# Kernel tuning notes

Measured on AMD Instinct MI355X. Metric: run time of the kernel, lower is better.

The kernel has to match this reference:

```python
import jax, jax.numpy as jnp
import numpy as np

B, L, D, H = 2, 2048, 1024, 16
DH = D // H  # 64

def setup_inputs() -> dict:
    key = jax.random.key(0)
    ks = jax.random.split(key, 5)
    s = 1.0 / np.sqrt(D)
    return {
        "x": jax.random.normal(ks[0], (B, L, D), jnp.float32),
        "Wk": jax.random.normal(ks[1], (D, D), jnp.float32) * s,
        "Wq": jax.random.normal(ks[2], (D, D), jnp.float32) * s,
        "Wv": jax.random.normal(ks[3], (D, D), jnp.float32) * s,
        "Wo": jax.random.normal(ks[4], (D, D), jnp.float32) * s,
    }

def reference(x, Wk, Wq, Wv, Wo):
    # Linear(D,D,bias=False): y = x @ W.T ; W stored [out,in] as in torch
    k = (x @ Wk.T).reshape(B, L, H, DH).transpose(0, 2, 1, 3)  # [B,H,L,dh]
    q = (x @ Wq.T).reshape(B, L, H, DH).transpose(0, 2, 1, 3)
    v = (x @ Wv.T).reshape(B, L, H, DH).transpose(0, 2, 1, 3)
    att = jnp.einsum("bhqd,bhkd->bhqk", q, k) / jnp.sqrt(jnp.float32(DH))
    causal = jnp.tril(jnp.ones((L, L), dtype=bool))
    att = jnp.where(causal, att, -jnp.inf)
    p = jax.nn.softmax(att, axis=-1)  # dropout omitted (eval mode)
    out = jnp.einsum("bhqk,bhkd->bhqd", p, v)  # [B,H,L,dh]
    out = out.transpose(0, 2, 1, 3).reshape(B, L, D)
    return out @ Wo.T
```

## Files before the change

### kernel.cpp

```cpp
#include <hip/hip_runtime.h>

typedef __bf16 bf16_t;
typedef __bf16 bf16x8 __attribute__((ext_vector_type(8)));
typedef __bf16 bf16x4 __attribute__((ext_vector_type(4)));
typedef float f32x4 __attribute__((ext_vector_type(4)));

#define MFMA_BF16(a, b, c) __builtin_amdgcn_mfma_f32_16x16x32_bf16((a), (b), (c), 0, 0, 0)
#define LOG2E 1.44269504088896f

__device__ __forceinline__ void gload16(const bf16_t* g, bf16_t* l) {
  __builtin_amdgcn_global_load_lds(
      (__attribute__((address_space(1))) void*)(g),
      (__attribute__((address_space(3))) void*)(l), 16, 0, 0);
}

__global__ void cast_all(const float* __restrict__ x, const float* __restrict__ wk,
                         const float* __restrict__ wq, const float* __restrict__ wv,
                         const float* __restrict__ wo, bf16_t* __restrict__ xbf,
                         bf16_t* __restrict__ wbf) {
  const size_t NX = 4194304, NW = 1048576;
  size_t i = (size_t)blockIdx.x * blockDim.x + threadIdx.x;
  const size_t total4 = (NX + 4 * NW) / 4;
  const size_t stride = (size_t)gridDim.x * blockDim.x;
  for (; i < total4; i += stride) {
    size_t f = i * 4;
    const float* src;
    bf16_t* dst;
    if (f < NX) {
      src = x + f;
      dst = xbf + f;
    } else {
      size_t g = f - NX;
      size_t wsel = g >> 20;
      size_t off = g & (NW - 1);
      dst = wbf + g;
      src = (wsel == 0) ? wq + off : (wsel == 1) ? wk + off : (wsel == 2) ? wv + off : wo + off;
    }
    float4 v = *(const float4*)src;
    bf16x4 o;
    o[0] = (bf16_t)v.x; o[1] = (bf16_t)v.y; o[2] = (bf16_t)v.z; o[3] = (bf16_t)v.w;
    *(bf16x4*)dst = o;
  }
}

template <int BM, int BN, typename TOUT>
__global__ __launch_bounds__(256) void gemm_nt(const bf16_t* __restrict__ A,
                                               const bf16_t* __restrict__ W,
                                               TOUT* __restrict__ C, int K, int ldc,
                                               int blocksPerSect, bf16_t* __restrict__ vtb) {
  constexpr int MF = BM / 32;
  constexpr int NF = BN / 32;
  __shared__ bf16_t As[BM * 32];
  __shared__ bf16_t Bs[BN * 32];
  const int t = threadIdx.x;
  const int l = t & 63, w = t >> 6;
  const int wm = w >> 1;
  const int wn = w & 1;
  const int lr = l & 15, lg = l >> 4;
  const int bm = blockIdx.x;
  const int by = blockIdx.y;
  const int sect = by / blocksPerSect;
  const int bn = by - sect * blocksPerSect;
  const bf16_t* Wp = W + ((size_t)sect << 20);
  const int n0 = sect * 1024 + bn * BN;

  const bf16_t* ag = A + (size_t)(bm * BM + (t >> 2)) * K + (t & 3) * 8;
  const bf16_t* bg = Wp + (size_t)(bn * BN + (t >> 2)) * K + (t & 3) * 8;
  const size_t rs64 = (size_t)64 * K;

  f32x4 acc[MF][NF];
#pragma unroll
  for (int i = 0; i < MF; ++i)
#pragma unroll
    for (int j = 0; j < NF; ++j) acc[i][j] = (f32x4){0.f, 0.f, 0.f, 0.f};

  for (int k0 = 0; k0 < K; k0 += 32) {
    __syncthreads();
    gload16(ag, As + t * 8);
    if (BM == 128) gload16(ag + rs64, As + 2048 + t * 8);
    gload16(bg, Bs + t * 8);
    if (BN == 128) gload16(bg + rs64, Bs + 2048 + t * 8);
    ag += 32;
    bg += 32;
    __syncthreads();
    bf16x8 af[MF], bfr[NF];
#pragma unroll
    for (int mf = 0; mf < MF; ++mf)
      af[mf] = *(const bf16x8*)(As + (wm * (MF * 16) + mf * 16 + lr) * 32 + lg * 8);
#pragma unroll
    for (int nf = 0; nf < NF; ++nf)
      bfr[nf] = *(const bf16x8*)(Bs + (wn * (NF * 16) + nf * 16 + lr) * 32 + lg * 8);
#pragma unroll
    for (int mf = 0; mf < MF; ++mf)
#pragma unroll
      for (int nf = 0; nf < NF; ++nf)
        acc[mf][nf] = MFMA_BF16(af[mf], bfr[nf], acc[mf][nf]);
  }

  if constexpr (BM == 128 && BN == 128) {
    if (vtb != nullptr && sect == 2) {
#pragma unroll
      for (int mf = 0; mf < MF; ++mf)
#pragma unroll
        for (int nf = 0; nf < NF; ++nf) {
          int row0 = bm * 128 + wm * 64 + mf * 16 + lg * 4;
          int colg = bn * 128 + wn * 64 + nf * 16 + lr;
          int bb = row0 >> 11, ll = row0 & 2047;
          size_t vaddr = ((size_t)((bb * 16 + (colg >> 6)) * 64 + (colg & 63))) * 2048 + ll;
          bf16x4 pk;
#pragma unroll
          for (int j = 0; j < 4; ++j) pk[j] = (bf16_t)acc[mf][nf][j];
          *(bf16x4*)(vtb + vaddr) = pk;
        }
      return;
    }
  }
#pragma unroll
  for (int mf = 0; mf < MF; ++mf)
#pragma unroll
    for (int nf = 0; nf < NF; ++nf)
#pragma unroll
      for (int j = 0; j < 4; ++j) {
        int row = bm * BM + wm * (MF * 16) + mf * 16 + lg * 4 + j;
        int col = n0 + wn * (NF * 16) + nf * 16 + lr;
        C[(size_t)row * ldc + col] = (TOUT)acc[mf][nf][j];
      }
}

__global__ __launch_bounds__(256) void attn_fwd(const bf16_t* __restrict__ qk,
                                                const bf16_t* __restrict__ vt,
                                                bf16_t* __restrict__ out) {
  __shared__ bf16_t Ks[2][4096];
  __shared__ bf16_t Vts[2][4096];
  __shared__ bf16_t Pt[4][1024];
  const int t = threadIdx.x, l = t & 63, w = t >> 6;
  const int lr = l & 15, lg = l >> 4;
  const int n = blockIdx.x;
  const int bh = n & 31;
  const int b = bh >> 4, h = bh & 15;
  const int m = n >> 5;
  const int j8 = m & 7, kk = m >> 3;
  const int qt = (kk == 0) ? j8 : (kk == 1) ? 15 - j8 : (kk == 2) ? 16 + j8 : 31 - j8;
  const int qloc = w * 16 + lr;
  const int qrow = qt * 64 + qloc;

  const float SCINIT = -12.f * LOG2E;

  const int srow = t >> 3, sc8 = t & 7;
  const int cs = sc8 ^ (srow & 7);
  const bf16_t* kbase = qk + ((size_t)(b * 2048 + srow)) * 2048 + 1024 + h * 64 + cs * 8;
  const bf16_t* vbase = vt + ((size_t)(bh * 64 + srow)) * 2048 + cs * 8;

#define STAGE(ktile, buf)                                              \
  do {                                                                 \
    const bf16_t* ks_ = kbase + (size_t)(ktile) * (64 * 2048);         \
    const bf16_t* vs_ = vbase + (size_t)(ktile) * 64;                  \
    gload16(ks_, &Ks[buf][t * 8]);                                     \
    gload16(ks_ + (size_t)32 * 2048, &Ks[buf][2048 + t * 8]);          \
    gload16(vs_, &Vts[buf][t * 8]);                                    \
    gload16(vs_ + (size_t)32 * 2048, &Vts[buf][2048 + t * 8]);         \
  } while (0)

  const float qsc = 0.125f * LOG2E;
  const bf16_t* Qg = qk + (size_t)(b * 2048 + qrow) * 2048 + h * 64 + lg * 8;
  bf16x8 qf0 = *(const bf16x8*)(Qg);
  bf16x8 qf1 = *(const bf16x8*)(Qg + 32);
#pragma unroll
  for (int jj = 0; jj < 8; ++jj) {
    qf0[jj] = (bf16_t)((float)qf0[jj] * qsc);
    qf1[jj] = (bf16_t)((float)qf1[jj] * qsc);
  }

  f32x4 acc[4];
#pragma unroll
  for (int df = 0; df < 4; ++df) acc[df] = (f32x4){0.f, 0.f, 0.f, 0.f};
  float l_r = 0.f;

  char* PwB = (char*)&Pt[w][0];
  const int psw = (lr & 7) << 4;

  STAGE(0, 0);
  __syncthreads();

  int cur = 0;
  for (int kt = 0; kt <= qt; ++kt) {
    if (kt < qt) STAGE(kt + 1, cur ^ 1);

    f32x4 sc[4];
#pragma unroll
    for (int nf = 0; nf < 4; ++nf)
      sc[nf] = (f32x4){SCINIT, SCINIT, SCINIT, SCINIT};
    __builtin_amdgcn_s_setprio(1);
#pragma unroll
    for (int nf = 0; nf < 4; ++nf) {
      int row = nf * 16 + lr, r7 = row & 7;
      bf16x8 kf0 = *(const bf16x8*)(&Ks[cur][row * 64 + (lg ^ r7) * 8]);
      bf16x8 kf1 = *(const bf16x8*)(&Ks[cur][row * 64 + ((lg ^ 4) ^ r7) * 8]);
      sc[nf] = MFMA_BF16(kf0, qf0, sc[nf]);
      sc[nf] = MFMA_BF16(kf1, qf1, sc[nf]);
    }
    __builtin_amdgcn_s_setprio(0);

    float s[16];
#pragma unroll
    for (int nf = 0; nf < 4; ++nf)
#pragma unroll
      for (int jj = 0; jj < 4; ++jj) s[nf * 4 + jj] = sc[nf][jj];
    if (kt == qt) {
#pragma unroll
      for (int nf = 0; nf < 4; ++nf)
#pragma unroll
        for (int jj = 0; jj < 4; ++jj)
          if (nf * 16 + lg * 4 + jj > qloc) s[nf * 4 + jj] = -1e30f;
    }

    float p[16], ps = 0.f;
#pragma unroll
    for (int i = 0; i < 16; ++i) {
      p[i] = __builtin_amdgcn_exp2f(s[i]);
      ps += p[i];
    }
    l_r += ps;

#pragma unroll
    for (int nf = 0; nf < 4; ++nf) {
      bf16x4 pk;
#pragma unroll
      for (int jj = 0; jj < 4; ++jj) pk[jj] = (bf16_t)p[nf * 4 + jj];
      *(bf16x4*)(PwB + lr * 128 + ((nf * 32 + lg * 8) ^ psw)) = pk;
    }

    bf16x8 pb0 = *(const bf16x8*)(PwB + lr * 128 + ((lg * 16) ^ psw));
    bf16x8 pb1 = *(const bf16x8*)(PwB + lr * 128 + ((64 + lg * 16) ^ psw));
    __builtin_amdgcn_s_setprio(1);
#pragma unroll
    for (int df = 0; df < 4; ++df) {
      int arow = df * 16 + lr, r7 = arow & 7;
      bf16x8 vf0 = *(const bf16x8*)(&Vts[cur][arow * 64 + (lg ^ r7) * 8]);
      bf16x8 vf1 = *(const bf16x8*)(&Vts[cur][arow * 64 + ((lg ^ 4) ^ r7) * 8]);
      acc[df] = MFMA_BF16(vf0, pb0, acc[df]);
      acc[df] = MFMA_BF16(vf1, pb1, acc[df]);
    }
    __builtin_amdgcn_s_setprio(0);
    __syncthreads();
    cur ^= 1;
  }
#undef STAGE

  l_r += __shfl_xor(l_r, 16);
  l_r += __shfl_xor(l_r, 32);
  float inv = 1.f / l_r;
#pragma unroll
  for (int df = 0; df < 4; ++df) {
    bf16x4 o;
#pragma unroll
    for (int jj = 0; jj < 4; ++jj) o[jj] = (bf16_t)(acc[df][jj] * inv);
    *(bf16x4*)(out + (size_t)(b * 2048 + qrow) * 1024 + h * 64 + df * 16 + lg * 4) = o;
  }
}

extern "C" void kernel_launch(void* const* d_in, const int* in_sizes, int n_in,
                              void* d_out, int out_size, void* d_ws, size_t ws_size,
                              hipStream_t stream) {
  const float* x = (const float*)d_in[0];
  const float* wk = (const float*)d_in[1];
  const float* wq = (const float*)d_in[2];
  const float* wv = (const float*)d_in[3];
  const float* wo = (const float*)d_in[4];

  bf16_t* xbf = (bf16_t*)d_ws;
  bf16_t* wbf = xbf + 4194304;
  bf16_t* qkbf = wbf + 4194304;
  bf16_t* vtbuf = qkbf + 8388608;
  bf16_t* attnbf = xbf;
  float* out = (float*)d_out;

  cast_all<<<dim3(2048), dim3(256), 0, stream>>>(x, wk, wq, wv, wo, xbf, wbf);
  gemm_nt<128, 128, bf16_t><<<dim3(32, 24), dim3(256), 0, stream>>>(xbf, wbf, qkbf, 1024, 2048, 8,
                                                                    vtbuf);
  attn_fwd<<<dim3(1024), dim3(256), 0, stream>>>(qkbf, vtbuf, attnbf);
  gemm_nt<64, 64, float><<<dim3(64, 16), dim3(256), 0, stream>>>(attnbf, wbf + 3 * 1048576, out,
                                                                 1024, 1024, 16, (bf16_t*)nullptr);
}
```

Baseline: 108.0 us.

## Use BK=64 with XOR-swizzled LDS tiles and 128x64 QKV GEMM tiles

The GEMM k-step is doubled from 32 to 64, halving the number of barrier pairs per tile. LDS rows use an XOR swizzle on the 16-byte chunk index to avoid bank conflicts on the MFMA fragment reads. The QKV projection switches from 128x128 to 128x64 tiles, doubling the grid to 1536 blocks for better CU occupancy at the cost of more A reloads. The V-transpose epilogue is generalized so it works with any tile size.

```diff
diff --git a/kernel.cpp b/kernel.cpp
--- a/kernel.cpp
+++ b/kernel.cpp
@@ -50,8 +50,8 @@
                                                int blocksPerSect, bf16_t* __restrict__ vtb) {
   constexpr int MF = BM / 32;
   constexpr int NF = BN / 32;
-  __shared__ bf16_t As[BM * 32];
-  __shared__ bf16_t Bs[BN * 32];
+  __shared__ bf16_t As[BM * 64];
+  __shared__ bf16_t Bs[BN * 64];
   const int t = threadIdx.x;
   const int l = t & 63, w = t >> 6;
   const int wm = w >> 1;
@@ -64,9 +64,10 @@
   const bf16_t* Wp = W + ((size_t)sect << 20);
   const int n0 = sect * 1024 + bn * BN;
 
-  const bf16_t* ag = A + (size_t)(bm * BM + (t >> 2)) * K + (t & 3) * 8;
-  const bf16_t* bg = Wp + (size_t)(bn * BN + (t >> 2)) * K + (t & 3) * 8;
-  const size_t rs64 = (size_t)64 * K;
+  const int srow0 = t >> 3;
+  const int csw = (t & 7) ^ (srow0 & 7);
+  const bf16_t* ag = A + (size_t)(bm * BM + srow0) * K + csw * 8;
+  const bf16_t* bg = Wp + (size_t)(bn * BN + srow0) * K + csw * 8;
 
   f32x4 acc[MF][NF];
 #pragma unroll
@@ -74,46 +75,51 @@
 #pragma unroll
     for (int j = 0; j < NF; ++j) acc[i][j] = (f32x4){0.f, 0.f, 0.f, 0.f};
 
-  for (int k0 = 0; k0 < K; k0 += 32) {
+  for (int k0 = 0; k0 < K; k0 += 64) {
     __syncthreads();
-    gload16(ag, As + t * 8);
-    if (BM == 128) gload16(ag + rs64, As + 2048 + t * 8);
-    gload16(bg, Bs + t * 8);
-    if (BN == 128) gload16(bg + rs64, Bs + 2048 + t * 8);
-    ag += 32;
-    bg += 32;
+#pragma unroll
+    for (int p = 0; p < BM / 32; ++p) gload16(ag + (size_t)(32 * p) * K, As + t * 8 + p * 2048);
+#pragma unroll
+    for (int p = 0; p < BN / 32; ++p) gload16(bg + (size_t)(32 * p) * K, Bs + t * 8 + p * 2048);
+    ag += 64;
+    bg += 64;
     __syncthreads();
-    bf16x8 af[MF], bfr[NF];
+#pragma unroll
+    for (int kk = 0; kk < 2; ++kk) {
+      bf16x8 af[MF], bfr[NF];
+#pragma unroll
+      for (int mf = 0; mf < MF; ++mf) {
+        int row = wm * (MF * 16) + mf * 16 + lr;
+        af[mf] = *(const bf16x8*)(As + row * 64 + (((kk * 4 + lg) ^ (row & 7)) * 8));
+      }
+#pragma unroll
+      for (int nf = 0; nf < NF; ++nf) {
+        int row = wn * (NF * 16) + nf * 16 + lr;
+        bfr[nf] = *(const bf16x8*)(Bs + row * 64 + (((kk * 4 + lg) ^ (row & 7)) * 8));
+      }
+#pragma unroll
+      for (int mf = 0; mf < MF; ++mf)
+#pragma unroll
+        for (int nf = 0; nf < NF; ++nf)
+          acc[mf][nf] = MFMA_BF16(af[mf], bfr[nf], acc[mf][nf]);
+    }
+  }
+
+  if (vtb != nullptr && sect == 2) {
 #pragma unroll
     for (int mf = 0; mf < MF; ++mf)
-      af[mf] = *(const bf16x8*)(As + (wm * (MF * 16) + mf * 16 + lr) * 32 + lg * 8);
-#pragma unroll
-    for (int nf = 0; nf < NF; ++nf)
-      bfr[nf] = *(const bf16x8*)(Bs + (wn * (NF * 16) + nf * 16 + lr) * 32 + lg * 8);
-#pragma unroll
-    for (int mf = 0; mf < MF; ++mf)
-#pragma unroll
-      for (int nf = 0; nf < NF; ++nf)
-        acc[mf][nf] = MFMA_BF16(af[mf], bfr[nf], acc[mf][nf]);
-  }
-
-  if constexpr (BM == 128 && BN == 128) {
-    if (vtb != nullptr && sect == 2) {
-#pragma unroll
-      for (int mf = 0; mf < MF; ++mf)
-#pragma unroll
-        for (int nf = 0; nf < NF; ++nf) {
-          int row0 = bm * 128 + wm * 64 + mf * 16 + lg * 4;
-          int colg = bn * 128 + wn * 64 + nf * 16 + lr;
-          int bb = row0 >> 11, ll = row0 & 2047;
-          size_t vaddr = ((size_t)((bb * 16 + (colg >> 6)) * 64 + (colg & 63))) * 2048 + ll;
-          bf16x4 pk;
-#pragma unroll
-          for (int j = 0; j < 4; ++j) pk[j] = (bf16_t)acc[mf][nf][j];
-          *(bf16x4*)(vtb + vaddr) = pk;
-        }
-      return;
-    }
+#pragma unroll
+      for (int nf = 0; nf < NF; ++nf) {
+        int row0 = bm * BM + wm * (MF * 16) + mf * 16 + lg * 4;
+        int colg = bn * BN + wn * (NF * 16) + nf * 16 + lr;
+        int bb = row0 >> 11, ll = row0 & 2047;
+        size_t vaddr = ((size_t)((bb * 16 + (colg >> 6)) * 64 + (colg & 63))) * 2048 + ll;
+        bf16x4 pk;
+#pragma unroll
+        for (int j = 0; j < 4; ++j) pk[j] = (bf16_t)acc[mf][nf][j];
+        *(bf16x4*)(vtb + vaddr) = pk;
+      }
+    return;
   }
 #pragma unroll
   for (int mf = 0; mf < MF; ++mf)
@@ -276,8 +282,8 @@
   float* out = (float*)d_out;
 
   cast_all<<<dim3(2048), dim3(256), 0, stream>>>(x, wk, wq, wv, wo, xbf, wbf);
-  gemm_nt<128, 128, bf16_t><<<dim3(32, 24), dim3(256), 0, stream>>>(xbf, wbf, qkbf, 1024, 2048, 8,
-                                                                    vtbuf);
+  gemm_nt<128, 64, bf16_t><<<dim3(32, 48), dim3(256), 0, stream>>>(xbf, wbf, qkbf, 1024, 2048, 16,
+                                                                   vtbuf);
   attn_fwd<<<dim3(1024), dim3(256), 0, stream>>>(qkbf, vtbuf, attnbf);
   gemm_nt<64, 64, float><<<dim3(64, 16), dim3(256), 0, stream>>>(attnbf, wbf + 3 * 1048576, out,
                                                                  1024, 1024, 16, (bf16_t*)nullptr);
```

Result: faster. 105.3 us (-2.5%).
